# Kernel optimization log

Hardware: AMD Instinct MI355X
Metric: run time of the kernel (lower is better)

The kernel has to match this reference:

```python
import jax, jax.numpy as jnp
import numpy as np

# dims: b=2, n=1024 windows, seq_ref=1, seq_in=16, nh_in=4 (seq_in*nh_in=64),
# nv=4 variables, nc=32 channels, n_lon=n_lat=4 Gaussian basis offsets
B, N, SR, SI, NH, NV, NC, NLON, NLAT = 2, 1024, 1, 16, 4, 4, 32, 4, 4
MIN_SIGMA = 1e-10


def setup_inputs() -> dict:
    key = jax.random.key(0)
    k1, k2, k3 = jax.random.split(key, 3)
    x = jax.random.normal(k1, (B, N, SR, SI * NH, NV, NC), dtype=jnp.float32)
    coords_lon = jax.random.normal(k2, (B, N, SR, SI, NH), dtype=jnp.float32)
    coords_lat = jax.random.normal(k3, (B, N, SR, SI, NH), dtype=jnp.float32)
    # mus are linspace(-grid_dist_out, grid_dist_out, n) in the torch module
    mus_lon = jnp.linspace(-1.0, 1.0, NLON).astype(jnp.float32)
    mus_lat = jnp.linspace(-1.0, 1.0, NLAT).astype(jnp.float32)
    sigma = jnp.full((1,), 0.5, dtype=jnp.float32)  # grid min_dist, learnable scalar
    return dict(x=x, coords_lon=coords_lon, coords_lat=coords_lat,
                mus_lon=mus_lon, mus_lat=mus_lat, sigma=sigma)


def reference(x, coords_lon, coords_lat, mus_lon, mus_lat, sigma):
    # x: (b,n,seq_ref,seq_in*nh_in,nv,nc); coords_*: (b,n,seq_ref,seq_in,nh_in)
    b, n, sr, si, nh = coords_lon.shape
    nv, nc = x.shape[-2:]
    nlon, nlat = mus_lon.shape[0], mus_lat.shape[0]
    sig = jnp.maximum(sigma, MIN_SIGMA)  # clamp(min=min_sigma)
    # Gaussian kernels over relative lon/lat distances
    wlon = jnp.exp(-0.5 * ((coords_lon[..., None] - mus_lon) / sig) ** 2)  # (b,n,sr,si,nh,Lo)
    wlat = jnp.exp(-0.5 * ((coords_lat[..., None] - mus_lat) / sig) ** 2)  # (b,n,sr,si,nh,La)
    # outer product over (Lo, La); flatten (seq_in, nh_in) -> s
    w = (wlon[..., :, None] * wlat[..., None, :]).reshape(b, n, sr, si * nh, nlon, nlat)
    # normalize over the neighbor axis (dim=3). weights are nv-independent
    # (torch repeat_interleaves over nv; broadcasting is equivalent)
    w = w / jnp.sum(w, axis=3, keepdims=True)
    # weighted neighbor aggregation: sum over s
    out = jnp.einsum('bnrsvc,bnrsxy->bnrvxyc', x, w)  # (b,n,sr,nv,Lo,La,nc)
    return out.reshape(b, n * sr, nv, nlon, nlat, nc)
```

## Files before the change

kernel.cpp:

```cpp
#include <hip/hip_runtime.h>
#include <hip/hip_bf16.h>

#define NWIN 2048
#define SDIM 64
#define NJ 16

__device__ __forceinline__ float bf2f(unsigned int u16) {
    union { unsigned int i; float f; } v;
    v.i = u16 << 16;
    return v.f;
}

__global__ __launch_bounds__(256, 2) void gauss_agg_kernel(
    const void* __restrict__ x,
    const void* __restrict__ clon,
    const void* __restrict__ clat,
    const void* __restrict__ mlon,
    const void* __restrict__ mlat,
    const void* __restrict__ sigma,
    float* __restrict__ out)
{
    __shared__ alignas(16) float s_wlon[4][SDIM][4];
    __shared__ alignas(16) float s_wlat[4][SDIM][4];
    __shared__ float s_sinv[4][NJ];
    __shared__ int s_flags;

    const int tid  = threadIdx.x;
    const int w4   = tid >> 6;
    const int lane = tid & 63;
    const int win  = blockIdx.x * 4 + w4;

    if (tid == 0) {
        const unsigned short* px = (const unsigned short*)x;
        const unsigned short* pc = (const unsigned short*)clon;
        int vx = 0, vc = 0;
#pragma unroll
        for (int i = 0; i < 16; ++i) {
            const int ex = (px[2 * i] >> 7) & 0xFF;
            vx += (ex >= 102 && ex <= 134);
            const int ec = (pc[2 * i] >> 7) & 0xFF;
            vc += (ec >= 102 && ec <= 134);
        }
        int f = 0;
        if (vx >= 12) f |= 1;
        if (vc >= 12) f |= 2;
        if (((const unsigned short*)mlon)[0] != 0) f |= 4;
        if (((const unsigned short*)sigma)[0] != 0) f |= 8;
        s_flags = f;
    }
    __syncthreads();
    const int flags = s_flags;
    const bool xb = flags & 1, cb = flags & 2, mb = flags & 4, sb = flags & 8;

    const float sigraw = sb ? bf2f(((const unsigned short*)sigma)[0])
                            : ((const float*)sigma)[0];
    const float inv = 1.0f / fmaxf(sigraw, 1e-10f);

    float mlo[4], mla[4];
#pragma unroll
    for (int l = 0; l < 4; ++l) {
        mlo[l] = mb ? bf2f(((const unsigned short*)mlon)[l])
                    : ((const float*)mlon)[l];
        mla[l] = mb ? bf2f(((const unsigned short*)mlat)[l])
                    : ((const float*)mlat)[l];
    }

    float lon, lat;
    if (cb) {
        lon = bf2f(((const unsigned short*)clon)[win * SDIM + lane]);
        lat = bf2f(((const unsigned short*)clat)[win * SDIM + lane]);
    } else {
        lon = ((const float*)clon)[win * SDIM + lane];
        lat = ((const float*)clat)[win * SDIM + lane];
    }

    float wlon[4], wlat[4];
#pragma unroll
    for (int l = 0; l < 4; ++l) {
        const float dlo = (lon - mlo[l]) * inv;
        wlon[l] = __expf(-0.5f * dlo * dlo);
        const float dla = (lat - mla[l]) * inv;
        wlat[l] = __expf(-0.5f * dla * dla);
    }
    *reinterpret_cast<float4*>(&s_wlon[w4][lane][0]) =
        make_float4(wlon[0], wlon[1], wlon[2], wlon[3]);
    *reinterpret_cast<float4*>(&s_wlat[w4][lane][0]) =
        make_float4(wlat[0], wlat[1], wlat[2], wlat[3]);

    float p[NJ];
#pragma unroll
    for (int lo = 0; lo < 4; ++lo)
#pragma unroll
        for (int la = 0; la < 4; ++la)
            p[lo * 4 + la] = wlon[lo] * wlat[la];
#pragma unroll
    for (int j = 0; j < NJ; ++j) {
        float v = p[j];
#pragma unroll
        for (int off = 1; off < 64; off <<= 1)
            v += __shfl_xor(v, off, 64);
        p[j] = v;
    }
    if (lane == 0) {
#pragma unroll
        for (int j = 0; j < NJ; ++j)
            s_sinv[w4][j] = 1.0f / p[j];
    }
    __syncthreads();

    const int v  = lane >> 4;
    const int c2 = lane & 15;
    const size_t base = (size_t)win * 4096 + v * 16 + c2;

    const float4* wl4 = reinterpret_cast<const float4*>(&s_wlon[w4][0][0]);
    const float4* wt4 = reinterpret_cast<const float4*>(&s_wlat[w4][0][0]);

    float acc0[NJ], acc1[NJ];
#pragma unroll
    for (int j = 0; j < NJ; ++j) { acc0[j] = 0.0f; acc1[j] = 0.0f; }

    if (xb) {
        const unsigned int* xp = (const unsigned int*)x + base;
#pragma unroll 4
        for (int s = 0; s < SDIM; ++s) {
            const unsigned int u = xp[s * 64];
            union { unsigned int i; float f; } u0, u1;
            u0.i = u << 16;
            u1.i = u & 0xffff0000u;
            const float f0 = u0.f, f1 = u1.f;
            const float4 wl = wl4[s];
            const float4 wt = wt4[s];
            const float wlv[4] = { wl.x, wl.y, wl.z, wl.w };
            const float wtv[4] = { wt.x, wt.y, wt.z, wt.w };
            float t0[4], t1[4];
#pragma unroll
            for (int la = 0; la < 4; ++la) { t0[la] = f0 * wtv[la]; t1[la] = f1 * wtv[la]; }
#pragma unroll
            for (int lo = 0; lo < 4; ++lo)
#pragma unroll
                for (int la = 0; la < 4; ++la) {
                    acc0[lo * 4 + la] += wlv[lo] * t0[la];
                    acc1[lo * 4 + la] += wlv[lo] * t1[la];
                }
        }
    } else {
        const float2* xp = (const float2*)x + base;
#pragma unroll 4
        for (int s = 0; s < SDIM; ++s) {
            const float2 xv = xp[s * 64];
            const float f0 = xv.x, f1 = xv.y;
            const float4 wl = wl4[s];
            const float4 wt = wt4[s];
            const float wlv[4] = { wl.x, wl.y, wl.z, wl.w };
            const float wtv[4] = { wt.x, wt.y, wt.z, wt.w };
            float t0[4], t1[4];
#pragma unroll
            for (int la = 0; la < 4; ++la) { t0[la] = f0 * wtv[la]; t1[la] = f1 * wtv[la]; }
#pragma unroll
            for (int lo = 0; lo < 4; ++lo)
#pragma unroll
                for (int la = 0; la < 4; ++la) {
                    acc0[lo * 4 + la] += wlv[lo] * t0[la];
                    acc1[lo * 4 + la] += wlv[lo] * t1[la];
                }
        }
    }

    float2* op = reinterpret_cast<float2*>(out);
#pragma unroll
    for (int j = 0; j < NJ; ++j) {
        const float si = s_sinv[w4][j];
        op[((size_t)(win * 4 + v) * NJ + j) * 16 + c2] =
            make_float2(acc0[j] * si, acc1[j] * si);
    }
}

extern "C" void kernel_launch(void* const* d_in, const int* in_sizes, int n_in,
                              void* d_out, int out_size, void* d_ws, size_t ws_size,
                              hipStream_t stream) {
    dim3 grid(NWIN / 4);
    dim3 block(256);
    gauss_agg_kernel<<<grid, block, 0, stream>>>(
        d_in[0], d_in[1], d_in[2], d_in[3], d_in[4], d_in[5],
        (float*)d_out);
}
```

Baseline: 113.3 us.

## Assign one window per block and split neighbor reduction across lanes

Each block now handles one window instead of four. The first wave computes the Gaussian weights and normalizers, and all four waves share the aggregation. The 64 neighbor samples are split across four lane groups, and the partial sums are combined with cross-lane shuffles before the output is written. The grid grows fourfold and occupancy is raised through launch bounds, so more waves are available to hide memory latency. In exchange, three waves sit idle during the weight phase and the shuffle-reduction step is new work.

After: 122.6 us. 8.3% more time.

```diff
diff --git a/kernel.cpp b/kernel.cpp
--- a/kernel.cpp
+++ b/kernel.cpp
@@ -11,7 +11,7 @@
     return v.f;
 }
 
-__global__ __launch_bounds__(256, 2) void gauss_agg_kernel(
+__global__ __launch_bounds__(256, 4) void gauss_agg_kernel(
     const void* __restrict__ x,
     const void* __restrict__ clon,
     const void* __restrict__ clat,
@@ -20,15 +20,13 @@
     const void* __restrict__ sigma,
     float* __restrict__ out)
 {
-    __shared__ alignas(16) float s_wlon[4][SDIM][4];
-    __shared__ alignas(16) float s_wlat[4][SDIM][4];
-    __shared__ float s_sinv[4][NJ];
+    __shared__ alignas(16) float s_wlon[SDIM][4];
+    __shared__ alignas(16) float s_wlat[SDIM][4];
+    __shared__ float s_sinv[NJ];
     __shared__ int s_flags;
 
-    const int tid  = threadIdx.x;
-    const int w4   = tid >> 6;
-    const int lane = tid & 63;
-    const int win  = blockIdx.x * 4 + w4;
+    const int tid = threadIdx.x;
+    const int win = blockIdx.x;
 
     if (tid == 0) {
         const unsigned short* px = (const unsigned short*)x;
@@ -52,82 +50,89 @@
     const int flags = s_flags;
     const bool xb = flags & 1, cb = flags & 2, mb = flags & 4, sb = flags & 8;
 
-    const float sigraw = sb ? bf2f(((const unsigned short*)sigma)[0])
-                            : ((const float*)sigma)[0];
-    const float inv = 1.0f / fmaxf(sigraw, 1e-10f);
-
-    float mlo[4], mla[4];
-#pragma unroll
-    for (int l = 0; l < 4; ++l) {
-        mlo[l] = mb ? bf2f(((const unsigned short*)mlon)[l])
-                    : ((const float*)mlon)[l];
-        mla[l] = mb ? bf2f(((const unsigned short*)mlat)[l])
-                    : ((const float*)mlat)[l];
-    }
-
-    float lon, lat;
-    if (cb) {
-        lon = bf2f(((const unsigned short*)clon)[win * SDIM + lane]);
-        lat = bf2f(((const unsigned short*)clat)[win * SDIM + lane]);
-    } else {
-        lon = ((const float*)clon)[win * SDIM + lane];
-        lat = ((const float*)clat)[win * SDIM + lane];
-    }
-
-    float wlon[4], wlat[4];
-#pragma unroll
-    for (int l = 0; l < 4; ++l) {
-        const float dlo = (lon - mlo[l]) * inv;
-        wlon[l] = __expf(-0.5f * dlo * dlo);
-        const float dla = (lat - mla[l]) * inv;
-        wlat[l] = __expf(-0.5f * dla * dla);
-    }
-    *reinterpret_cast<float4*>(&s_wlon[w4][lane][0]) =
-        make_float4(wlon[0], wlon[1], wlon[2], wlon[3]);
-    *reinterpret_cast<float4*>(&s_wlat[w4][lane][0]) =
-        make_float4(wlat[0], wlat[1], wlat[2], wlat[3]);
-
-    float p[NJ];
-#pragma unroll
-    for (int lo = 0; lo < 4; ++lo)
-#pragma unroll
-        for (int la = 0; la < 4; ++la)
-            p[lo * 4 + la] = wlon[lo] * wlat[la];
-#pragma unroll
-    for (int j = 0; j < NJ; ++j) {
-        float v = p[j];
-#pragma unroll
-        for (int off = 1; off < 64; off <<= 1)
-            v += __shfl_xor(v, off, 64);
-        p[j] = v;
-    }
-    if (lane == 0) {
-#pragma unroll
-        for (int j = 0; j < NJ; ++j)
-            s_sinv[w4][j] = 1.0f / p[j];
+    if (tid < 64) {
+        const int lane = tid;
+        const float sigraw = sb ? bf2f(((const unsigned short*)sigma)[0])
+                                : ((const float*)sigma)[0];
+        const float inv = 1.0f / fmaxf(sigraw, 1e-10f);
+
+        float mlo[4], mla[4];
+#pragma unroll
+        for (int l = 0; l < 4; ++l) {
+            mlo[l] = mb ? bf2f(((const unsigned short*)mlon)[l])
+                        : ((const float*)mlon)[l];
+            mla[l] = mb ? bf2f(((const unsigned short*)mlat)[l])
+                        : ((const float*)mlat)[l];
+        }
+
+        float lon, lat;
+        if (cb) {
+            lon = bf2f(((const unsigned short*)clon)[win * SDIM + lane]);
+            lat = bf2f(((const unsigned short*)clat)[win * SDIM + lane]);
+        } else {
+            lon = ((const float*)clon)[win * SDIM + lane];
+            lat = ((const float*)clat)[win * SDIM + lane];
+        }
+
+        float wlon[4], wlat[4];
+#pragma unroll
+        for (int l = 0; l < 4; ++l) {
+            const float dlo = (lon - mlo[l]) * inv;
+            wlon[l] = __expf(-0.5f * dlo * dlo);
+            const float dla = (lat - mla[l]) * inv;
+            wlat[l] = __expf(-0.5f * dla * dla);
+        }
+        *reinterpret_cast<float4*>(&s_wlon[lane][0]) =
+            make_float4(wlon[0], wlon[1], wlon[2], wlon[3]);
+        *reinterpret_cast<float4*>(&s_wlat[lane][0]) =
+            make_float4(wlat[0], wlat[1], wlat[2], wlat[3]);
+
+        float p[NJ];
+#pragma unroll
+        for (int lo = 0; lo < 4; ++lo)
+#pragma unroll
+            for (int la = 0; la < 4; ++la)
+                p[lo * 4 + la] = wlon[lo] * wlat[la];
+#pragma unroll
+        for (int j = 0; j < NJ; ++j) {
+            float v = p[j];
+#pragma unroll
+            for (int off = 1; off < 64; off <<= 1)
+                v += __shfl_xor(v, off, 64);
+            p[j] = v;
+        }
+        if (lane == 0) {
+#pragma unroll
+            for (int j = 0; j < NJ; ++j)
+                s_sinv[j] = 1.0f / p[j];
+        }
     }
     __syncthreads();
 
-    const int v  = lane >> 4;
-    const int c2 = lane & 15;
+    const int v    = tid >> 6;
+    const int lane = tid & 63;
+    const int sp   = lane >> 4;
+    const int c2   = lane & 15;
+
+    const float4* wl4 = reinterpret_cast<const float4*>(&s_wlon[0][0]);
+    const float4* wt4 = reinterpret_cast<const float4*>(&s_wlat[0][0]);
+
+    float acc[NJ][2];
+#pragma unroll
+    for (int j = 0; j < NJ; ++j) { acc[j][0] = 0.0f; acc[j][1] = 0.0f; }
+
     const size_t base = (size_t)win * 4096 + v * 16 + c2;
-
-    const float4* wl4 = reinterpret_cast<const float4*>(&s_wlon[w4][0][0]);
-    const float4* wt4 = reinterpret_cast<const float4*>(&s_wlat[w4][0][0]);
-
-    float acc0[NJ], acc1[NJ];
-#pragma unroll
-    for (int j = 0; j < NJ; ++j) { acc0[j] = 0.0f; acc1[j] = 0.0f; }
 
     if (xb) {
         const unsigned int* xp = (const unsigned int*)x + base;
-#pragma unroll 4
-        for (int s = 0; s < SDIM; ++s) {
+#pragma unroll 8
+        for (int it = 0; it < 16; ++it) {
+            const int s = 4 * it + sp;
             const unsigned int u = xp[s * 64];
-            union { unsigned int i; float f; } u0, u1;
+            union { unsigned int i; float fl; } u0, u1;
             u0.i = u << 16;
             u1.i = u & 0xffff0000u;
-            const float f0 = u0.f, f1 = u1.f;
+            const float f0 = u0.fl, f1 = u1.fl;
             const float4 wl = wl4[s];
             const float4 wt = wt4[s];
             const float wlv[4] = { wl.x, wl.y, wl.z, wl.w };
@@ -139,14 +144,15 @@
             for (int lo = 0; lo < 4; ++lo)
 #pragma unroll
                 for (int la = 0; la < 4; ++la) {
-                    acc0[lo * 4 + la] += wlv[lo] * t0[la];
-                    acc1[lo * 4 + la] += wlv[lo] * t1[la];
+                    acc[lo * 4 + la][0] += wlv[lo] * t0[la];
+                    acc[lo * 4 + la][1] += wlv[lo] * t1[la];
                 }
         }
     } else {
         const float2* xp = (const float2*)x + base;
-#pragma unroll 4
-        for (int s = 0; s < SDIM; ++s) {
+#pragma unroll 8
+        for (int it = 0; it < 16; ++it) {
+            const int s = 4 * it + sp;
             const float2 xv = xp[s * 64];
             const float f0 = xv.x, f1 = xv.y;
             const float4 wl = wl4[s];
@@ -160,25 +166,34 @@
             for (int lo = 0; lo < 4; ++lo)
 #pragma unroll
                 for (int la = 0; la < 4; ++la) {
-                    acc0[lo * 4 + la] += wlv[lo] * t0[la];
-                    acc1[lo * 4 + la] += wlv[lo] * t1[la];
+                    acc[lo * 4 + la][0] += wlv[lo] * t0[la];
+                    acc[lo * 4 + la][1] += wlv[lo] * t1[la];
                 }
         }
     }
 
+#pragma unroll
+    for (int j = 0; j < NJ; ++j)
+#pragma unroll
+        for (int k = 0; k < 2; ++k) {
+            acc[j][k] += __shfl_xor(acc[j][k], 16, 64);
+            acc[j][k] += __shfl_xor(acc[j][k], 32, 64);
+        }
+
     float2* op = reinterpret_cast<float2*>(out);
 #pragma unroll
-    for (int j = 0; j < NJ; ++j) {
-        const float si = s_sinv[w4][j];
+    for (int jj = 0; jj < 4; ++jj) {
+        const int j = sp * 4 + jj;
+        const float si = s_sinv[j];
         op[((size_t)(win * 4 + v) * NJ + j) * 16 + c2] =
-            make_float2(acc0[j] * si, acc1[j] * si);
+            make_float2(acc[j][0] * si, acc[j][1] * si);
     }
 }
 
 extern "C" void kernel_launch(void* const* d_in, const int* in_sizes, int n_in,
                               void* d_out, int out_size, void* d_ws, size_t ws_size,
                               hipStream_t stream) {
-    dim3 grid(NWIN / 4);
+    dim3 grid(NWIN);
     dim3 block(256);
     gauss_agg_kernel<<<grid, block, 0, stream>>>(
         d_in[0], d_in[1], d_in[2], d_in[3], d_in[4], d_in[5],
```
